# Kernel optimization log

Measured on AMD Instinct MI355X. Metric: run time of the kernel, lower is better.

## Reference

```python
import jax, jax.numpy as jnp
import numpy as np
from jax import lax

B_, C_, H_, W_ = 4, 128, 64, 64
D_INNER, D_STATE, DT_RANK, D_CONV = 256, 16, 8, 4


def setup_inputs() -> dict:
    ks = jax.random.split(jax.random.key(0), 12)
    def rn(k, shape, fan_in):
        return jax.random.normal(k, shape, jnp.float32) * (fan_in ** -0.5)
    return {
        "x": jax.random.normal(ks[0], (B_, C_, H_, W_), jnp.float32),
        "proj_w": rn(ks[1], (C_, C_), C_),
        "in_proj_w": rn(ks[2], (2 * D_INNER, C_), C_),
        "conv_w": rn(ks[3], (D_INNER, 1, D_CONV), D_CONV),
        "conv_b": jax.random.normal(ks[4], (D_INNER,), jnp.float32) * 0.02,
        "x_proj_w": rn(ks[5], (DT_RANK + 2 * D_STATE, D_INNER), D_INNER),
        "dt_proj_w": rn(ks[6], (D_INNER, DT_RANK), DT_RANK),
        "dt_proj_b": jax.random.normal(ks[7], (D_INNER,), jnp.float32) * 0.1,
        "A_log": jax.random.uniform(ks[8], (D_INNER, D_STATE), jnp.float32),
        "D": jax.random.normal(ks[9], (D_INNER,), jnp.float32),
        "out_proj_w": rn(ks[10], (C_, D_INNER), D_INNER),
    }


def _mamba2d(x, proj_w, in_proj_w, conv_w, conv_b, x_proj_w, dt_proj_w, dt_proj_b, A_log, D, out_proj_w):
    b, c, h, w = x.shape
    L = h * w
    # 1x1 conv projection then flatten to sequence (b, L, c)
    u = jnp.einsum('oc,bchw->bohw', proj_w, x).reshape(b, c, L).transpose(0, 2, 1)
    # in_proj -> x, z gates
    xz = u @ in_proj_w.T                      # (b, L, 2*d_inner)
    xs, zg = xz[..., :D_INNER], xz[..., D_INNER:]
    # causal depthwise conv1d over sequence
    xt = xs.transpose(0, 2, 1)                # (b, d_inner, L)
    xt = lax.conv_general_dilated(xt, conv_w, window_strides=(1,),
                                  padding=[(D_CONV - 1, 0)],
                                  feature_group_count=D_INNER)
    xc = jax.nn.silu(xt + conv_b[None, :, None]).transpose(0, 2, 1)  # (b, L, d_inner)
    # input-dependent SSM params
    x_dbl = xc @ x_proj_w.T                   # (b, L, dt_rank + 2*d_state)
    dt_r = x_dbl[..., :DT_RANK]
    Bm = x_dbl[..., DT_RANK:DT_RANK + D_STATE]
    Cm = x_dbl[..., DT_RANK + D_STATE:]
    delta = jax.nn.softplus(dt_r @ dt_proj_w.T + dt_proj_b)  # (b, L, d_inner)
    A = -jnp.exp(A_log)                       # (d_inner, d_state)

    def step(hprev, inp):
        dt_t, B_t, C_t, x_t = inp             # (b,d), (b,n), (b,n), (b,d)
        dA = jnp.exp(dt_t[:, :, None] * A)    # (b, d, n)
        hn = dA * hprev + (dt_t * x_t)[:, :, None] * B_t[:, None, :]
        y = jnp.einsum('bdn,bn->bd', hn, C_t)
        return hn, y

    h0 = jnp.zeros((b, D_INNER, D_STATE), xc.dtype)
    _, ys = lax.scan(step, h0, (delta.transpose(1, 0, 2), Bm.transpose(1, 0, 2),
                                Cm.transpose(1, 0, 2), xc.transpose(1, 0, 2)))
    y = ys.transpose(1, 0, 2) + xc * D        # (b, L, d_inner) + skip
    y = y * jax.nn.silu(zg)                   # output gating
    out = y @ out_proj_w.T                    # (b, L, c)
    return out.transpose(0, 2, 1).reshape(b, c, h, w) + x


def reference(x, proj_w, in_proj_w, conv_w, conv_b, x_proj_w, dt_proj_w, dt_proj_b, A_log, D, out_proj_w):
    return _mamba2d(x, proj_w, in_proj_w, conv_w, conv_b, x_proj_w, dt_proj_w, dt_proj_b, A_log, D, out_proj_w)
```

## Files before the change

### kernel.cpp

```cpp
#include <hip/hip_runtime.h>


#define NCHUNK 128
#define CLEN 32

using s16x8 = __attribute__((ext_vector_type(8))) short;
using f32x4 = __attribute__((ext_vector_type(4))) float;

__device__ inline unsigned short f2bf(float f) {
  unsigned u = __float_as_uint(f);
  u = u + 0x7FFF + ((u >> 16) & 1);
  return (unsigned short)(u >> 16);
}
__device__ inline float bfu(unsigned short v) {
  return __uint_as_float((unsigned)v << 16);
}

__global__ void prep_kernel(const float* __restrict__ proj_w,
                            const float* __restrict__ in_proj_w,
                            const float* __restrict__ x_proj_w,
                            const float* __restrict__ out_proj_w,
                            const float* __restrict__ A_log,
                            unsigned short* __restrict__ W2b,
                            unsigned short* __restrict__ wTb48,
                            unsigned short* __restrict__ Woutb,
                            float* __restrict__ Aneg) {
  int idx = blockIdx.x * blockDim.x + threadIdx.x;
  if (idx < 65536) {
    int o = idx >> 7, c = idx & 127;
    float acc = 0.f;
    #pragma unroll 4
    for (int i = 0; i < 128; ++i)
      acc += in_proj_w[o * 128 + i] * proj_w[i * 128 + c];
    W2b[idx] = f2bf(acc);
  } else if (idx < 65536 + 12288) {
    int t = idx - 65536;
    int j = t >> 8, k = t & 255;
    wTb48[t] = (j < 40) ? f2bf(x_proj_w[j * 256 + k]) : (unsigned short)0;
  } else if (idx < 65536 + 12288 + 32768) {
    int t = idx - (65536 + 12288);
    Woutb[t] = f2bf(out_proj_w[t]);
  } else if (idx < 65536 + 12288 + 32768 + 4096) {
    int t = idx - (65536 + 12288 + 32768);
    Aneg[t] = -__expf(A_log[t]);
  }
}

__global__ __launch_bounds__(256, 1) void gemm_xz_kernel(
    const float* __restrict__ x, const unsigned short* __restrict__ W2b,
    unsigned short* __restrict__ xT, unsigned short* __restrict__ zT) {
  __shared__ __align__(16) unsigned short At[128 * 128];
  __shared__ __align__(16) unsigned short Bt[256 * 128];
  int m0 = (blockIdx.x >> 1) * 128;
  int o0 = (blockIdx.x & 1) * 256;
  int b  = m0 >> 12;
  int l0 = m0 & 4095;
  int t = threadIdx.x;
  #pragma unroll
  for (int j = 0; j < 16; ++j) {
    int flat = t + j * 256;
    int cr = flat >> 5, lq = (flat & 31) << 2;
    float4 v = *reinterpret_cast<const float4*>(
        &x[((size_t)(b * 128 + cr)) * 4096 + l0 + lq]);
    float vv[4] = {v.x, v.y, v.z, v.w};
    #pragma unroll
    for (int e = 0; e < 4; ++e) {
      int l = lq + e;
      int g = (cr >> 3) ^ ((l & 7) << 1);
      At[l * 128 + g * 8 + (cr & 7)] = f2bf(vv[e]);
    }
  }
  #pragma unroll
  for (int j = 0; j < 16; ++j) {
    int flat = t + j * 256;
    int row = flat >> 4, gB = flat & 15;
    s16x8 v = *reinterpret_cast<const s16x8*>(&W2b[(size_t)(o0 + row) * 128 + gB * 8]);
    int g = gB ^ ((row & 7) << 1);
    *reinterpret_cast<s16x8*>(&Bt[row * 128 + g * 8]) = v;
  }
  __syncthreads();
  int ln = t & 63, wave = t >> 6;
  int wm = wave & 1, wn = wave >> 1;
  f32x4 acc[4][8] = {};
  #pragma unroll
  for (int ks = 0; ks < 4; ++ks) {
    int gk = ks * 4 + (ln >> 4);
    s16x8 a[4], bb[8];
    #pragma unroll
    for (int mi = 0; mi < 4; ++mi) {
      int lr = wm * 64 + mi * 16 + (ln & 15);
      a[mi] = *reinterpret_cast<const s16x8*>(&At[lr * 128 + (gk ^ ((lr & 7) << 1)) * 8]);
    }
    #pragma unroll
    for (int ni = 0; ni < 8; ++ni) {
      int orow = wn * 128 + ni * 16 + (ln & 15);
      bb[ni] = *reinterpret_cast<const s16x8*>(&Bt[orow * 128 + (gk ^ ((orow & 7) << 1)) * 8]);
    }
    #pragma unroll
    for (int mi = 0; mi < 4; ++mi)
      #pragma unroll
      for (int ni = 0; ni < 8; ++ni)
        acc[mi][ni] = __builtin_amdgcn_mfma_f32_16x16x32_bf16(a[mi], bb[ni], acc[mi][ni], 0, 0, 0);
  }
  unsigned short* T = (o0 == 0) ? xT : zT;
  #pragma unroll
  for (int mi = 0; mi < 4; ++mi)
    #pragma unroll
    for (int ni = 0; ni < 8; ++ni) {
      int colg = wn * 128 + ni * 16 + (ln & 15);
      int lrow = l0 + wm * 64 + mi * 16 + ((ln >> 4) << 2);
      ushort4 h4{f2bf(acc[mi][ni][0]), f2bf(acc[mi][ni][1]),
                 f2bf(acc[mi][ni][2]), f2bf(acc[mi][ni][3])};
      *reinterpret_cast<ushort4*>(&T[((size_t)(b * 256 + colg)) * 4096 + lrow]) = h4;
    }
}

__global__ __launch_bounds__(256) void conv_silu_kernel(
    const unsigned short* __restrict__ xT, const float* __restrict__ conv_w,
    const float* __restrict__ conv_b, unsigned short* __restrict__ xcT,
    unsigned short* __restrict__ xcb) {
  __shared__ unsigned short sxc[16][256];
  int blk = blockIdx.x;
  int b = blk >> 8, ch = blk & 255;
  int l0 = ch * 16;
  int d = threadIdx.x;
  size_t rowbase = ((size_t)(b * 256 + d)) * 4096;
  s16x8 w16[3];
  const s16x8* src = reinterpret_cast<const s16x8*>(&xT[rowbase + l0 - 8]);
  w16[0] = src[0]; w16[1] = src[1]; w16[2] = src[2];
  float wf[24];
  #pragma unroll
  for (int i = 0; i < 3; ++i)
    #pragma unroll
    for (int e = 0; e < 8; ++e)
      wf[i * 8 + e] = bfu((unsigned short)w16[i][e]);
  if (l0 == 0) { wf[5] = 0.f; wf[6] = 0.f; wf[7] = 0.f; }
  float w0 = conv_w[d * 4 + 0], w1 = conv_w[d * 4 + 1];
  float w2 = conv_w[d * 4 + 2], w3 = conv_w[d * 4 + 3];
  float cb = conv_b[d];
  unsigned short outv[16];
  #pragma unroll
  for (int r = 0; r < 16; ++r) {
    float acc = cb + w3 * wf[8 + r] + w2 * wf[7 + r] + w1 * wf[6 + r] + w0 * wf[5 + r];
    float s = acc * (1.f / (1.f + __expf(-acc)));
    unsigned short v = f2bf(s);
    outv[r] = v;
    sxc[r][d] = v;
  }
  #pragma unroll
  for (int i = 0; i < 2; ++i) {
    s16x8 v;
    #pragma unroll
    for (int e = 0; e < 8; ++e) v[e] = (short)outv[i * 8 + e];
    *reinterpret_cast<s16x8*>(&xcT[rowbase + l0 + i * 8]) = v;
  }
  __syncthreads();
  #pragma unroll
  for (int it = 0; it < 2; ++it) {
    int idx = d + it * 256;
    int l = idx >> 5, ds8 = (idx & 31) * 8;
    s16x8 v = *reinterpret_cast<const s16x8*>(&sxc[l][ds8]);
    *reinterpret_cast<s16x8*>(&xcb[((size_t)(b * 4096 + l0 + l)) * 256 + ds8]) = v;
  }
}

__global__ __launch_bounds__(256) void xdbl_mfma_kernel(
    const unsigned short* __restrict__ xcb, const unsigned short* __restrict__ wTb48,
    float* __restrict__ xdbl48) {
  __shared__ __align__(16) unsigned short At[64 * 256];
  __shared__ __align__(16) unsigned short Bt[48 * 256];
  int m0 = blockIdx.x * 64;
  int t = threadIdx.x;
  #pragma unroll
  for (int it = 0; it < 8; ++it) {
    int f = t + it * 256;
    int row = f >> 5, g0 = f & 31;
    s16x8 v = *reinterpret_cast<const s16x8*>(&xcb[(size_t)(m0 + row) * 256 + g0 * 8]);
    int g = g0 ^ ((row & 7) << 1);
    *reinterpret_cast<s16x8*>(&At[row * 256 + g * 8]) = v;
  }
  #pragma unroll
  for (int it = 0; it < 6; ++it) {
    int f = t + it * 256;
    int row = f >> 5, g0 = f & 31;
    s16x8 v = *reinterpret_cast<const s16x8*>(&wTb48[(size_t)row * 256 + g0 * 8]);
    int g = g0 ^ ((row & 7) << 1);
    *reinterpret_cast<s16x8*>(&Bt[row * 256 + g * 8]) = v;
  }
  __syncthreads();
  int ln = t & 63, wm = t >> 6;
  f32x4 acc[3] = {};
  #pragma unroll
  for (int ks = 0; ks < 8; ++ks) {
    int gk = ks * 4 + (ln >> 4);
    int ar = wm * 16 + (ln & 15);
    s16x8 a = *reinterpret_cast<const s16x8*>(&At[ar * 256 + (gk ^ ((ar & 7) << 1)) * 8]);
    #pragma unroll
    for (int nt = 0; nt < 3; ++nt) {
      int br = nt * 16 + (ln & 15);
      s16x8 bb = *reinterpret_cast<const s16x8*>(&Bt[br * 256 + (gk ^ ((br & 7) << 1)) * 8]);
      acc[nt] = __builtin_amdgcn_mfma_f32_16x16x32_bf16(a, bb, acc[nt], 0, 0, 0);
    }
  }
  #pragma unroll
  for (int nt = 0; nt < 3; ++nt)
    #pragma unroll
    for (int r = 0; r < 4; ++r) {
      int row = m0 + wm * 16 + (ln >> 4) * 4 + r;
      xdbl48[(size_t)row * 48 + nt * 16 + (ln & 15)] = acc[nt][r];
    }
}

__global__ __launch_bounds__(256) void scan1_kernel(
    const unsigned short* __restrict__ xcT, const float* __restrict__ xdbl48,
    const float* __restrict__ dt_proj_w, const float* __restrict__ dt_proj_b,
    const float* __restrict__ Aneg,
    float* __restrict__ Ssum, float* __restrict__ chH) {
  __shared__ __align__(16) float lBC[CLEN][32];
  __shared__ __align__(16) float sdtr[CLEN][8];
  int blk = blockIdx.x;
  int b = blk >> 7, c = blk & 127;
  int bl0 = blk * CLEN;
  int tid = threadIdx.x;
  {
    int t0 = tid >> 3, q = (tid & 7) << 2;
    *reinterpret_cast<float4*>(&lBC[t0][q]) =
        *reinterpret_cast<const float4*>(&xdbl48[(size_t)(bl0 + t0) * 48 + 8 + q]);
    if (tid < 64) {
      int t1 = tid >> 1, q1 = (tid & 1) << 2;
      *reinterpret_cast<float4*>(&sdtr[t1][q1]) =
          *reinterpret_cast<const float4*>(&xdbl48[(size_t)(bl0 + t1) * 48 + q1]);
    }
  }
  int d = tid;
  float wrow[8];
  *reinterpret_cast<float4*>(&wrow[0]) = *reinterpret_cast<const float4*>(&dt_proj_w[d * 8]);
  *reinterpret_cast<float4*>(&wrow[4]) = *reinterpret_cast<const float4*>(&dt_proj_w[d * 8 + 4]);
  float bb = dt_proj_b[d];
  float An[16];
  #pragma unroll
  for (int q = 0; q < 4; ++q)
    *reinterpret_cast<float4*>(&An[q * 4]) =
        *reinterpret_cast<const float4*>(&Aneg[d * 16 + q * 4]);
  s16x8 xw[4];
  {
    const s16x8* src = reinterpret_cast<const s16x8*>(
        &xcT[((size_t)(b * 256 + d)) * 4096 + c * CLEN]);
    xw[0] = src[0]; xw[1] = src[1]; xw[2] = src[2]; xw[3] = src[3];
  }
  __syncthreads();
  float h[16] = {};
  float S = 0.f;
  #pragma unroll
  for (int t = 0; t < CLEN; ++t) {
    float a = bb;
    #pragma unroll
    for (int q = 0; q < 8; ++q) a += sdtr[t][q] * wrow[q];
    float dlv = fmaxf(a, 0.f) + __logf(1.f + __expf(-fabsf(a)));
    S += dlv;
    float dlx = dlv * bfu((unsigned short)xw[t >> 3][t & 7]);
    #pragma unroll
    for (int n = 0; n < 16; ++n)
      h[n] = __expf(dlv * An[n]) * h[n] + dlx * lBC[t][n];
  }
  int p = b * 256 + d;
  Ssum[c * 1024 + p] = S;
  size_t base = ((size_t)(c * 1024 + p)) * 16;
  #pragma unroll
  for (int q = 0; q < 4; ++q) {
    float4 v{h[q*4+0], h[q*4+1], h[q*4+2], h[q*4+3]};
    *reinterpret_cast<float4*>(&chH[base + q * 4]) = v;
  }
}

__global__ void scan2_kernel(const float* __restrict__ Aneg,
                             const float* __restrict__ Ssum,
                             const float* __restrict__ chH,
                             float* __restrict__ chS) {
  int q = blockIdx.x * blockDim.x + threadIdx.x;
  int p = q >> 4, n = q & 15;
  int d = p & 255;
  float An = Aneg[d * 16 + n];
  float h = 0.f;
  #pragma unroll 8
  for (int c = 0; c < NCHUNK; ++c) {
    size_t idx = ((size_t)(c * 1024 + p)) * 16 + n;
    float S = Ssum[c * 1024 + p];
    float hl = chH[idx];
    chS[idx] = h;
    h = __expf(An * S) * h + hl;
  }
}

__global__ __launch_bounds__(256) void scan3_kernel(
    const unsigned short* __restrict__ xcT, const unsigned short* __restrict__ zT,
    const float* __restrict__ xdbl48,
    const float* __restrict__ dt_proj_w, const float* __restrict__ dt_proj_b,
    const float* __restrict__ Aneg, const float* __restrict__ chS,
    const float* __restrict__ Dvec, unsigned short* __restrict__ y2b) {
  __shared__ __align__(16) float lBC[CLEN][32];
  __shared__ __align__(16) float sdtr[CLEN][8];
  __shared__ unsigned short sy[CLEN][256];
  int blk = blockIdx.x;
  int b = blk >> 7, c = blk & 127;
  int bl0 = blk * CLEN;
  int tid = threadIdx.x;
  {
    int t0 = tid >> 3, q = (tid & 7) << 2;
    *reinterpret_cast<float4*>(&lBC[t0][q]) =
        *reinterpret_cast<const float4*>(&xdbl48[(size_t)(bl0 + t0) * 48 + 8 + q]);
    if (tid < 64) {
      int t1 = tid >> 1, q1 = (tid & 1) << 2;
      *reinterpret_cast<float4*>(&sdtr[t1][q1]) =
          *reinterpret_cast<const float4*>(&xdbl48[(size_t)(bl0 + t1) * 48 + q1]);
    }
  }
  int d = tid;
  float wrow[8];
  *reinterpret_cast<float4*>(&wrow[0]) = *reinterpret_cast<const float4*>(&dt_proj_w[d * 8]);
  *reinterpret_cast<float4*>(&wrow[4]) = *reinterpret_cast<const float4*>(&dt_proj_w[d * 8 + 4]);
  float bb = dt_proj_b[d];
  float An[16];
  #pragma unroll
  for (int q = 0; q < 4; ++q)
    *reinterpret_cast<float4*>(&An[q * 4]) =
        *reinterpret_cast<const float4*>(&Aneg[d * 16 + q * 4]);
  int p = b * 256 + d;
  float h[16];
  {
    size_t base = ((size_t)(c * 1024 + p)) * 16;
    #pragma unroll
    for (int q = 0; q < 4; ++q) {
      float4 v = *reinterpret_cast<const float4*>(&chS[base + q * 4]);
      h[q*4+0] = v.x; h[q*4+1] = v.y; h[q*4+2] = v.z; h[q*4+3] = v.w;
    }
  }
  s16x8 xw[4], zw[4];
  {
    size_t rb = ((size_t)(b * 256 + d)) * 4096 + c * CLEN;
    const s16x8* sx = reinterpret_cast<const s16x8*>(&xcT[rb]);
    const s16x8* sz = reinterpret_cast<const s16x8*>(&zT[rb]);
    xw[0] = sx[0]; xw[1] = sx[1]; xw[2] = sx[2]; xw[3] = sx[3];
    zw[0] = sz[0]; zw[1] = sz[1]; zw[2] = sz[2]; zw[3] = sz[3];
  }
  float Dd = Dvec[d];
  __syncthreads();
  #pragma unroll
  for (int t = 0; t < CLEN; ++t) {
    float a = bb;
    #pragma unroll
    for (int q = 0; q < 8; ++q) a += sdtr[t][q] * wrow[q];
    float dlv = fmaxf(a, 0.f) + __logf(1.f + __expf(-fabsf(a)));
    float xval = bfu((unsigned short)xw[t >> 3][t & 7]);
    float dlx = dlv * xval;
    float y = 0.f;
    #pragma unroll
    for (int n = 0; n < 16; ++n) {
      h[n] = __expf(dlv * An[n]) * h[n] + dlx * lBC[t][n];
      y += h[n] * lBC[t][16 + n];
    }
    float z = bfu((unsigned short)zw[t >> 3][t & 7]);
    float sil = z * (1.f / (1.f + __expf(-z)));
    sy[t][d] = f2bf((y + xval * Dd) * sil);
  }
  __syncthreads();
  #pragma unroll
  for (int it = 0; it < 4; ++it) {
    int idx = tid + it * 256;
    int l = idx >> 5, ds8 = (idx & 31) * 8;
    s16x8 v = *reinterpret_cast<const s16x8*>(&sy[l][ds8]);
    *reinterpret_cast<s16x8*>(&y2b[((size_t)(bl0 + l)) * 256 + ds8]) = v;
  }
}

__global__ __launch_bounds__(256) void gemm_out_kernel(
    const unsigned short* __restrict__ y2b, const unsigned short* __restrict__ Woutb,
    const float* __restrict__ x, float* __restrict__ out) {
  __shared__ __align__(16) unsigned short At[64 * 256];
  __shared__ __align__(16) unsigned short Bt[128 * 256];
  int m0 = blockIdx.x * 64;
  int b = m0 >> 12, l0 = m0 & 4095;
  int t = threadIdx.x;
  #pragma unroll
  for (int it = 0; it < 8; ++it) {
    int f = t + it * 256;
    int row = f >> 5, g0 = f & 31;
    s16x8 v = *reinterpret_cast<const s16x8*>(&y2b[(size_t)(m0 + row) * 256 + g0 * 8]);
    int g = g0 ^ ((row & 7) << 1);
    *reinterpret_cast<s16x8*>(&At[row * 256 + g * 8]) = v;
  }
  #pragma unroll
  for (int it = 0; it < 16; ++it) {
    int f = t + it * 256;
    int row = f >> 5, g0 = f & 31;
    s16x8 v = *reinterpret_cast<const s16x8*>(&Woutb[(size_t)row * 256 + g0 * 8]);
    int g = g0 ^ ((row & 7) << 1);
    *reinterpret_cast<s16x8*>(&Bt[row * 256 + g * 8]) = v;
  }
  __syncthreads();
  int ln = t & 63, wm = t >> 6;
  f32x4 acc[8] = {};
  #pragma unroll
  for (int ks = 0; ks < 8; ++ks) {
    int gk = ks * 4 + (ln >> 4);
    int ar = wm * 16 + (ln & 15);
    s16x8 a = *reinterpret_cast<const s16x8*>(&At[ar * 256 + (gk ^ ((ar & 7) << 1)) * 8]);
    #pragma unroll
    for (int nt = 0; nt < 8; ++nt) {
      int br = nt * 16 + (ln & 15);
      s16x8 bb = *reinterpret_cast<const s16x8*>(&Bt[br * 256 + (gk ^ ((br & 7) << 1)) * 8]);
      acc[nt] = __builtin_amdgcn_mfma_f32_16x16x32_bf16(a, bb, acc[nt], 0, 0, 0);
    }
  }
  #pragma unroll
  for (int nt = 0; nt < 8; ++nt) {
    int cc = nt * 16 + (ln & 15);
    size_t base = ((size_t)(b * 128 + cc)) * 4096 + l0 + wm * 16 + ((ln >> 4) << 2);
    float4 xr = *reinterpret_cast<const float4*>(&x[base]);
    float4 o{acc[nt][0] + xr.x, acc[nt][1] + xr.y, acc[nt][2] + xr.z, acc[nt][3] + xr.w};
    *reinterpret_cast<float4*>(&out[base]) = o;
  }
}

extern "C" void kernel_launch(void* const* d_in, const int* in_sizes, int n_in,
                              void* d_out, int out_size, void* d_ws, size_t ws_size,
                              hipStream_t stream) {
  const float* x         = (const float*)d_in[0];
  const float* proj_w    = (const float*)d_in[1];
  const float* in_proj_w = (const float*)d_in[2];
  const float* conv_w    = (const float*)d_in[3];
  const float* conv_b    = (const float*)d_in[4];
  const float* x_proj_w  = (const float*)d_in[5];
  const float* dt_proj_w = (const float*)d_in[6];
  const float* dt_proj_b = (const float*)d_in[7];
  const float* A_log     = (const float*)d_in[8];
  const float* Dvec      = (const float*)d_in[9];
  const float* out_proj_w= (const float*)d_in[10];

  float* ws = (float*)d_ws;
  float*          Aneg   = ws;
  unsigned short* W2b    = (unsigned short*)(ws + 4096);
  unsigned short* wTb48  = (unsigned short*)(ws + 36864);
  unsigned short* Woutb  = (unsigned short*)(ws + 43008);
  unsigned short* xT     = (unsigned short*)(ws + 59424);
  unsigned short* zT     = (unsigned short*)(ws + 2156576);
  unsigned short* xcT    = (unsigned short*)(ws + 4253728);
  unsigned short* xcb    = (unsigned short*)(ws + 6350880);
  float*          xdbl48 = ws + 8448032;
  float*          Ssum   = ws + 9234464;
  float*          chH    = ws + 9365536;
  float*          chS    = ws + 11462688;
  unsigned short* y2b    = (unsigned short*)(ws + 13559840);
  float* out = (float*)d_out;

  prep_kernel<<<448, 256, 0, stream>>>(proj_w, in_proj_w, x_proj_w, out_proj_w, A_log,
                                       W2b, wTb48, Woutb, Aneg);
  gemm_xz_kernel<<<256, 256, 0, stream>>>(x, W2b, xT, zT);
  conv_silu_kernel<<<1024, 256, 0, stream>>>(xT, conv_w, conv_b, xcT, xcb);
  xdbl_mfma_kernel<<<256, 256, 0, stream>>>(xcb, wTb48, xdbl48);
  scan1_kernel<<<512, 256, 0, stream>>>(xcT, xdbl48, dt_proj_w, dt_proj_b, Aneg,
                                        Ssum, chH);
  scan2_kernel<<<64, 256, 0, stream>>>(Aneg, Ssum, chH, chS);
  scan3_kernel<<<512, 256, 0, stream>>>(xcT, zT, xdbl48, dt_proj_w, dt_proj_b, Aneg,
                                        chS, Dvec, y2b);
  gemm_out_kernel<<<256, 256, 0, stream>>>(y2b, Woutb, x, out);
}
```

Measured before the change: 184.1 us.

## Fuse conv-SiLU, x_proj GEMM and chunk scan into one kernel; retile xz GEMM

Merges the depthwise conv+SiLU, the x_proj MFMA GEMM and the first chunked scan pass into a single mid_kernel. Each block handles one 32-token chunk, keeps xc in registers and shared memory, computes x_dbl with a split-K MFMA reduction in LDS, and runs the chunk scan directly. This removes the xcb intermediate and two kernel launches with their global round trips. The xz GEMM is retiled to 64-row blocks that loop over both output halves and no longer pin occupancy to one block per CU. scan2's launch shape also changes, and the larger LDS footprint of mid_kernel may reduce occupancy.

```diff
diff --git a/kernel.cpp b/kernel.cpp
--- a/kernel.cpp
+++ b/kernel.cpp
@@ -46,193 +46,165 @@
   }
 }
 
-__global__ __launch_bounds__(256, 1) void gemm_xz_kernel(
+__global__ __launch_bounds__(256) void gemm_xz_kernel(
     const float* __restrict__ x, const unsigned short* __restrict__ W2b,
     unsigned short* __restrict__ xT, unsigned short* __restrict__ zT) {
-  __shared__ __align__(16) unsigned short At[128 * 128];
+  __shared__ __align__(16) unsigned short At[64 * 128];
   __shared__ __align__(16) unsigned short Bt[256 * 128];
-  int m0 = (blockIdx.x >> 1) * 128;
-  int o0 = (blockIdx.x & 1) * 256;
-  int b  = m0 >> 12;
-  int l0 = m0 & 4095;
+  int blk = blockIdx.x;
+  int b = blk >> 6;
+  int l0 = (blk & 63) * 64;
   int t = threadIdx.x;
   #pragma unroll
-  for (int j = 0; j < 16; ++j) {
+  for (int j = 0; j < 8; ++j) {
     int flat = t + j * 256;
-    int cr = flat >> 5, lq = (flat & 31) << 2;
+    int c = flat >> 4, lq = (flat & 15) << 2;
     float4 v = *reinterpret_cast<const float4*>(
-        &x[((size_t)(b * 128 + cr)) * 4096 + l0 + lq]);
+        &x[((size_t)(b * 128 + c)) * 4096 + l0 + lq]);
     float vv[4] = {v.x, v.y, v.z, v.w};
     #pragma unroll
     for (int e = 0; e < 4; ++e) {
       int l = lq + e;
-      int g = (cr >> 3) ^ ((l & 7) << 1);
-      At[l * 128 + g * 8 + (cr & 7)] = f2bf(vv[e]);
-    }
-  }
-  #pragma unroll
-  for (int j = 0; j < 16; ++j) {
-    int flat = t + j * 256;
-    int row = flat >> 4, gB = flat & 15;
-    s16x8 v = *reinterpret_cast<const s16x8*>(&W2b[(size_t)(o0 + row) * 128 + gB * 8]);
-    int g = gB ^ ((row & 7) << 1);
-    *reinterpret_cast<s16x8*>(&Bt[row * 128 + g * 8]) = v;
-  }
-  __syncthreads();
-  int ln = t & 63, wave = t >> 6;
-  int wm = wave & 1, wn = wave >> 1;
-  f32x4 acc[4][8] = {};
-  #pragma unroll
-  for (int ks = 0; ks < 4; ++ks) {
-    int gk = ks * 4 + (ln >> 4);
-    s16x8 a[4], bb[8];
-    #pragma unroll
-    for (int mi = 0; mi < 4; ++mi) {
-      int lr = wm * 64 + mi * 16 + (ln & 15);
-      a[mi] = *reinterpret_cast<const s16x8*>(&At[lr * 128 + (gk ^ ((lr & 7) << 1)) * 8]);
-    }
-    #pragma unroll
-    for (int ni = 0; ni < 8; ++ni) {
-      int orow = wn * 128 + ni * 16 + (ln & 15);
-      bb[ni] = *reinterpret_cast<const s16x8*>(&Bt[orow * 128 + (gk ^ ((orow & 7) << 1)) * 8]);
-    }
-    #pragma unroll
-    for (int mi = 0; mi < 4; ++mi)
+      int g = (c >> 3) ^ ((l & 7) << 1);
+      At[l * 128 + g * 8 + (c & 7)] = f2bf(vv[e]);
+    }
+  }
+  int ln = t & 63, w = t >> 6;
+  for (int half = 0; half < 2; ++half) {
+    int o0 = half * 256;
+    __syncthreads();
+    #pragma unroll
+    for (int j = 0; j < 16; ++j) {
+      int flat = t + j * 256;
+      int row = flat >> 4, gB = flat & 15;
+      s16x8 v = *reinterpret_cast<const s16x8*>(&W2b[(size_t)(o0 + row) * 128 + gB * 8]);
+      int g = gB ^ ((row & 7) << 1);
+      *reinterpret_cast<s16x8*>(&Bt[row * 128 + g * 8]) = v;
+    }
+    __syncthreads();
+    f32x4 acc[16] = {};
+    #pragma unroll
+    for (int ks = 0; ks < 4; ++ks) {
+      int gk = ks * 4 + (ln >> 4);
+      int ar = w * 16 + (ln & 15);
+      s16x8 a = *reinterpret_cast<const s16x8*>(&At[ar * 128 + (gk ^ ((ar & 7) << 1)) * 8]);
       #pragma unroll
-      for (int ni = 0; ni < 8; ++ni)
-        acc[mi][ni] = __builtin_amdgcn_mfma_f32_16x16x32_bf16(a[mi], bb[ni], acc[mi][ni], 0, 0, 0);
-  }
-  unsigned short* T = (o0 == 0) ? xT : zT;
-  #pragma unroll
-  for (int mi = 0; mi < 4; ++mi)
-    #pragma unroll
-    for (int ni = 0; ni < 8; ++ni) {
-      int colg = wn * 128 + ni * 16 + (ln & 15);
-      int lrow = l0 + wm * 64 + mi * 16 + ((ln >> 4) << 2);
-      ushort4 h4{f2bf(acc[mi][ni][0]), f2bf(acc[mi][ni][1]),
-                 f2bf(acc[mi][ni][2]), f2bf(acc[mi][ni][3])};
-      *reinterpret_cast<ushort4*>(&T[((size_t)(b * 256 + colg)) * 4096 + lrow]) = h4;
-    }
-}
-
-__global__ __launch_bounds__(256) void conv_silu_kernel(
+      for (int nt = 0; nt < 16; ++nt) {
+        int br = nt * 16 + (ln & 15);
+        s16x8 bb = *reinterpret_cast<const s16x8*>(&Bt[br * 128 + (gk ^ ((br & 7) << 1)) * 8]);
+        acc[nt] = __builtin_amdgcn_mfma_f32_16x16x32_bf16(a, bb, acc[nt], 0, 0, 0);
+      }
+    }
+    unsigned short* T = half ? zT : xT;
+    #pragma unroll
+    for (int nt = 0; nt < 16; ++nt) {
+      int d = nt * 16 + (ln & 15);
+      int lrow = l0 + w * 16 + ((ln >> 4) << 2);
+      ushort4 h4{f2bf(acc[nt][0]), f2bf(acc[nt][1]), f2bf(acc[nt][2]), f2bf(acc[nt][3])};
+      *reinterpret_cast<ushort4*>(&T[((size_t)(b * 256 + d)) * 4096 + lrow]) = h4;
+    }
+  }
+}
+
+__global__ __launch_bounds__(256) void mid_kernel(
     const unsigned short* __restrict__ xT, const float* __restrict__ conv_w,
-    const float* __restrict__ conv_b, unsigned short* __restrict__ xcT,
-    unsigned short* __restrict__ xcb) {
-  __shared__ unsigned short sxc[16][256];
+    const float* __restrict__ conv_b, const unsigned short* __restrict__ wTb48,
+    const float* __restrict__ dt_proj_w, const float* __restrict__ dt_proj_b,
+    const float* __restrict__ Aneg,
+    unsigned short* __restrict__ xcT, float* __restrict__ xdbl48,
+    float* __restrict__ Ssum, float* __restrict__ chH) {
+  __shared__ __align__(16) unsigned short sxc[32 * 256];
+  __shared__ __align__(16) unsigned short sBt[48 * 256];
+  __shared__ __align__(16) float pxd[4 * 32 * 49];
   int blk = blockIdx.x;
-  int b = blk >> 8, ch = blk & 255;
-  int l0 = ch * 16;
+  int b = blk >> 7, c = blk & 127;
+  int l0 = c * CLEN;
+  int bl0 = blk * CLEN;
   int d = threadIdx.x;
   size_t rowbase = ((size_t)(b * 256 + d)) * 4096;
-  s16x8 w16[3];
-  const s16x8* src = reinterpret_cast<const s16x8*>(&xT[rowbase + l0 - 8]);
-  w16[0] = src[0]; w16[1] = src[1]; w16[2] = src[2];
-  float wf[24];
-  #pragma unroll
-  for (int i = 0; i < 3; ++i)
-    #pragma unroll
-    for (int e = 0; e < 8; ++e)
-      wf[i * 8 + e] = bfu((unsigned short)w16[i][e]);
-  if (l0 == 0) { wf[5] = 0.f; wf[6] = 0.f; wf[7] = 0.f; }
+  float wf[40];
+  {
+    const s16x8* src = reinterpret_cast<const s16x8*>(&xT[rowbase + l0 - 8]);
+    #pragma unroll
+    for (int i = 0; i < 5; ++i) {
+      s16x8 v = src[i];
+      #pragma unroll
+      for (int e = 0; e < 8; ++e) wf[i * 8 + e] = bfu((unsigned short)v[e]);
+    }
+    if (l0 == 0) { wf[5] = 0.f; wf[6] = 0.f; wf[7] = 0.f; }
+  }
   float w0 = conv_w[d * 4 + 0], w1 = conv_w[d * 4 + 1];
   float w2 = conv_w[d * 4 + 2], w3 = conv_w[d * 4 + 3];
   float cb = conv_b[d];
-  unsigned short outv[16];
-  #pragma unroll
-  for (int r = 0; r < 16; ++r) {
+  float xc[32];
+  unsigned short xcb16[32];
+  #pragma unroll
+  for (int r = 0; r < 32; ++r) {
     float acc = cb + w3 * wf[8 + r] + w2 * wf[7 + r] + w1 * wf[6 + r] + w0 * wf[5 + r];
     float s = acc * (1.f / (1.f + __expf(-acc)));
-    unsigned short v = f2bf(s);
-    outv[r] = v;
-    sxc[r][d] = v;
-  }
-  #pragma unroll
-  for (int i = 0; i < 2; ++i) {
+    xc[r] = s;
+    xcb16[r] = f2bf(s);
+  }
+  #pragma unroll
+  for (int i = 0; i < 4; ++i) {
     s16x8 v;
     #pragma unroll
-    for (int e = 0; e < 8; ++e) v[e] = (short)outv[i * 8 + e];
+    for (int e = 0; e < 8; ++e) v[e] = (short)xcb16[i * 8 + e];
     *reinterpret_cast<s16x8*>(&xcT[rowbase + l0 + i * 8]) = v;
   }
-  __syncthreads();
-  #pragma unroll
-  for (int it = 0; it < 2; ++it) {
-    int idx = d + it * 256;
-    int l = idx >> 5, ds8 = (idx & 31) * 8;
-    s16x8 v = *reinterpret_cast<const s16x8*>(&sxc[l][ds8]);
-    *reinterpret_cast<s16x8*>(&xcb[((size_t)(b * 4096 + l0 + l)) * 256 + ds8]) = v;
-  }
-}
-
-__global__ __launch_bounds__(256) void xdbl_mfma_kernel(
-    const unsigned short* __restrict__ xcb, const unsigned short* __restrict__ wTb48,
-    float* __restrict__ xdbl48) {
-  __shared__ __align__(16) unsigned short At[64 * 256];
-  __shared__ __align__(16) unsigned short Bt[48 * 256];
-  int m0 = blockIdx.x * 64;
-  int t = threadIdx.x;
-  #pragma unroll
-  for (int it = 0; it < 8; ++it) {
-    int f = t + it * 256;
-    int row = f >> 5, g0 = f & 31;
-    s16x8 v = *reinterpret_cast<const s16x8*>(&xcb[(size_t)(m0 + row) * 256 + g0 * 8]);
-    int g = g0 ^ ((row & 7) << 1);
-    *reinterpret_cast<s16x8*>(&At[row * 256 + g * 8]) = v;
-  }
+  #pragma unroll
+  for (int l = 0; l < 32; ++l)
+    sxc[l * 256 + (((d >> 3) ^ ((l & 7) << 1)) << 3) + (d & 7)] = xcb16[l];
   #pragma unroll
   for (int it = 0; it < 6; ++it) {
-    int f = t + it * 256;
+    int f = d + it * 256;
     int row = f >> 5, g0 = f & 31;
     s16x8 v = *reinterpret_cast<const s16x8*>(&wTb48[(size_t)row * 256 + g0 * 8]);
     int g = g0 ^ ((row & 7) << 1);
-    *reinterpret_cast<s16x8*>(&Bt[row * 256 + g * 8]) = v;
-  }
-  __syncthreads();
-  int ln = t & 63, wm = t >> 6;
-  f32x4 acc[3] = {};
-  #pragma unroll
-  for (int ks = 0; ks < 8; ++ks) {
-    int gk = ks * 4 + (ln >> 4);
-    int ar = wm * 16 + (ln & 15);
-    s16x8 a = *reinterpret_cast<const s16x8*>(&At[ar * 256 + (gk ^ ((ar & 7) << 1)) * 8]);
-    #pragma unroll
-    for (int nt = 0; nt < 3; ++nt) {
-      int br = nt * 16 + (ln & 15);
-      s16x8 bb = *reinterpret_cast<const s16x8*>(&Bt[br * 256 + (gk ^ ((br & 7) << 1)) * 8]);
-      acc[nt] = __builtin_amdgcn_mfma_f32_16x16x32_bf16(a, bb, acc[nt], 0, 0, 0);
-    }
-  }
-  #pragma unroll
-  for (int nt = 0; nt < 3; ++nt)
-    #pragma unroll
-    for (int r = 0; r < 4; ++r) {
-      int row = m0 + wm * 16 + (ln >> 4) * 4 + r;
-      xdbl48[(size_t)row * 48 + nt * 16 + (ln & 15)] = acc[nt][r];
-    }
-}
-
-__global__ __launch_bounds__(256) void scan1_kernel(
-    const unsigned short* __restrict__ xcT, const float* __restrict__ xdbl48,
-    const float* __restrict__ dt_proj_w, const float* __restrict__ dt_proj_b,
-    const float* __restrict__ Aneg,
-    float* __restrict__ Ssum, float* __restrict__ chH) {
-  __shared__ __align__(16) float lBC[CLEN][32];
-  __shared__ __align__(16) float sdtr[CLEN][8];
-  int blk = blockIdx.x;
-  int b = blk >> 7, c = blk & 127;
-  int bl0 = blk * CLEN;
-  int tid = threadIdx.x;
+    *reinterpret_cast<s16x8*>(&sBt[row * 256 + g * 8]) = v;
+  }
+  __syncthreads();
   {
-    int t0 = tid >> 3, q = (tid & 7) << 2;
-    *reinterpret_cast<float4*>(&lBC[t0][q]) =
-        *reinterpret_cast<const float4*>(&xdbl48[(size_t)(bl0 + t0) * 48 + 8 + q]);
-    if (tid < 64) {
-      int t1 = tid >> 1, q1 = (tid & 1) << 2;
-      *reinterpret_cast<float4*>(&sdtr[t1][q1]) =
-          *reinterpret_cast<const float4*>(&xdbl48[(size_t)(bl0 + t1) * 48 + q1]);
-    }
-  }
-  int d = tid;
+    int ln = d & 63, w = d >> 6;
+    f32x4 acc[2][3] = {};
+    #pragma unroll
+    for (int kk = 0; kk < 2; ++kk) {
+      int ks = w * 2 + kk;
+      int gk = ks * 4 + (ln >> 4);
+      #pragma unroll
+      for (int m = 0; m < 2; ++m) {
+        int ar = m * 16 + (ln & 15);
+        s16x8 a = *reinterpret_cast<const s16x8*>(&sxc[ar * 256 + (gk ^ ((ar & 7) << 1)) * 8]);
+        #pragma unroll
+        for (int nt = 0; nt < 3; ++nt) {
+          int br = nt * 16 + (ln & 15);
+          s16x8 bb = *reinterpret_cast<const s16x8*>(&sBt[br * 256 + (gk ^ ((br & 7) << 1)) * 8]);
+          acc[m][nt] = __builtin_amdgcn_mfma_f32_16x16x32_bf16(a, bb, acc[m][nt], 0, 0, 0);
+        }
+      }
+    }
+    #pragma unroll
+    for (int m = 0; m < 2; ++m)
+      #pragma unroll
+      for (int nt = 0; nt < 3; ++nt)
+        #pragma unroll
+        for (int r = 0; r < 4; ++r) {
+          int row = m * 16 + (ln >> 4) * 4 + r;
+          int col = nt * 16 + (ln & 15);
+          pxd[(w * 32 + row) * 49 + col] = acc[m][nt][r];
+        }
+  }
+  __syncthreads();
+  #pragma unroll
+  for (int it = 0; it < 6; ++it) {
+    int idx = d + it * 256;
+    int l = idx / 48, j = idx - l * 48;
+    float s = pxd[l * 49 + j] + pxd[(32 + l) * 49 + j] +
+              pxd[(64 + l) * 49 + j] + pxd[(96 + l) * 49 + j];
+    pxd[l * 49 + j] = s;
+    xdbl48[(size_t)blk * 1536 + idx] = s;
+  }
+  __syncthreads();
   float wrow[8];
   *reinterpret_cast<float4*>(&wrow[0]) = *reinterpret_cast<const float4*>(&dt_proj_w[d * 8]);
   *reinterpret_cast<float4*>(&wrow[4]) = *reinterpret_cast<const float4*>(&dt_proj_w[d * 8 + 4]);
@@ -242,26 +214,19 @@
   for (int q = 0; q < 4; ++q)
     *reinterpret_cast<float4*>(&An[q * 4]) =
         *reinterpret_cast<const float4*>(&Aneg[d * 16 + q * 4]);
-  s16x8 xw[4];
-  {
-    const s16x8* src = reinterpret_cast<const s16x8*>(
-        &xcT[((size_t)(b * 256 + d)) * 4096 + c * CLEN]);
-    xw[0] = src[0]; xw[1] = src[1]; xw[2] = src[2]; xw[3] = src[3];
-  }
-  __syncthreads();
   float h[16] = {};
   float S = 0.f;
   #pragma unroll
   for (int t = 0; t < CLEN; ++t) {
     float a = bb;
     #pragma unroll
-    for (int q = 0; q < 8; ++q) a += sdtr[t][q] * wrow[q];
+    for (int q = 0; q < 8; ++q) a += pxd[t * 49 + q] * wrow[q];
     float dlv = fmaxf(a, 0.f) + __logf(1.f + __expf(-fabsf(a)));
     S += dlv;
-    float dlx = dlv * bfu((unsigned short)xw[t >> 3][t & 7]);
+    float dlx = dlv * xc[t];
     #pragma unroll
     for (int n = 0; n < 16; ++n)
-      h[n] = __expf(dlv * An[n]) * h[n] + dlx * lBC[t][n];
+      h[n] = __expf(dlv * An[n]) * h[n] + dlx * pxd[t * 49 + 8 + n];
   }
   int p = b * 256 + d;
   Ssum[c * 1024 + p] = S;
@@ -445,22 +410,19 @@
   unsigned short* xT     = (unsigned short*)(ws + 59424);
   unsigned short* zT     = (unsigned short*)(ws + 2156576);
   unsigned short* xcT    = (unsigned short*)(ws + 4253728);
-  unsigned short* xcb    = (unsigned short*)(ws + 6350880);
-  float*          xdbl48 = ws + 8448032;
-  float*          Ssum   = ws + 9234464;
-  float*          chH    = ws + 9365536;
-  float*          chS    = ws + 11462688;
-  unsigned short* y2b    = (unsigned short*)(ws + 13559840);
+  float*          xdbl48 = ws + 6350880;
+  float*          Ssum   = ws + 7137312;
+  float*          chH    = ws + 7268384;
+  float*          chS    = ws + 9365536;
+  unsigned short* y2b    = (unsigned short*)(ws + 11462688);
   float* out = (float*)d_out;
 
   prep_kernel<<<448, 256, 0, stream>>>(proj_w, in_proj_w, x_proj_w, out_proj_w, A_log,
                                        W2b, wTb48, Woutb, Aneg);
   gemm_xz_kernel<<<256, 256, 0, stream>>>(x, W2b, xT, zT);
-  conv_silu_kernel<<<1024, 256, 0, stream>>>(xT, conv_w, conv_b, xcT, xcb);
-  xdbl_mfma_kernel<<<256, 256, 0, stream>>>(xcb, wTb48, xdbl48);
-  scan1_kernel<<<512, 256, 0, stream>>>(xcT, xdbl48, dt_proj_w, dt_proj_b, Aneg,
-                                        Ssum, chH);
-  scan2_kernel<<<64, 256, 0, stream>>>(Aneg, Ssum, chH, chS);
+  mid_kernel<<<512, 256, 0, stream>>>(xT, conv_w, conv_b, wTb48, dt_proj_w, dt_proj_b,
+                                      Aneg, xcT, xdbl48, Ssum, chH);
+  scan2_kernel<<<128, 128, 0, stream>>>(Aneg, Ssum, chH, chS);
   scan3_kernel<<<512, 256, 0, stream>>>(xcT, zT, xdbl48, dt_proj_w, dt_proj_b, Aneg,
                                         chS, Dvec, y2b);
   gemm_out_kernel<<<256, 256, 0, stream>>>(y2b, Woutb, x, out);
```

Result: faster. 178.0 us (-3.3%).
